# Kernel tuning notes

Measured on AMD Instinct MI355X. Metric: run time of the kernel, lower is better.

The kernel has to match this reference:

```python
import jax, jax.numpy as jnp
import numpy as np

B, S, HID = 1, 2048, 2048
H, KV, D = 16, 4, 128
N_REP = H // KV
WINDOW = 1024
THETA = 10000.0
EPS = 1e-6
SCALE = D ** -0.5


def setup_inputs() -> dict:
    key = jax.random.key(0)
    ks = jax.random.split(key, 10)
    s = 0.02
    return {
        "hidden_states": jax.random.normal(ks[0], (B, S, HID), jnp.float32),
        "Wq": jax.random.normal(ks[1], (HID, H * D), jnp.float32) * s,
        "bq": jnp.zeros((H * D,), jnp.float32),
        "Wk": jax.random.normal(ks[2], (HID, KV * D), jnp.float32) * s,
        "bk": jnp.zeros((KV * D,), jnp.float32),
        "Wv": jax.random.normal(ks[3], (HID, KV * D), jnp.float32) * s,
        "bv": jnp.zeros((KV * D,), jnp.float32),
        "Wo": jax.random.normal(ks[4], (H * D, HID), jnp.float32) * s,
        "memory_gate": jnp.zeros((1, H, 1, 1), jnp.float32),
    }


def _rope_tables(seq_len, dim, dtype):
    inv_freq = 1.0 / (THETA ** (jnp.arange(0, dim, 2, dtype=jnp.float32) / dim))
    t = jnp.arange(seq_len, dtype=jnp.float32)
    freqs = t[:, None] * inv_freq[None, :]          # [S, D/2]
    emb = jnp.concatenate([freqs, freqs], axis=-1)  # [S, D]
    return jnp.cos(emb).astype(dtype), jnp.sin(emb).astype(dtype)


def _rotate_half(x):
    x1, x2 = x[..., : x.shape[-1] // 2], x[..., x.shape[-1] // 2 :]
    return jnp.concatenate([-x2, x1], axis=-1)


def reference(hidden_states, Wq, bq, Wk, bk, Wv, bv, Wo, memory_gate):
    b, s, _ = hidden_states.shape
    q = (hidden_states @ Wq + bq).reshape(b, s, H, D).transpose(0, 2, 1, 3)   # [B,H,S,D]
    k = (hidden_states @ Wk + bk).reshape(b, s, KV, D).transpose(0, 2, 1, 3)  # [B,KV,S,D]
    v = (hidden_states @ Wv + bv).reshape(b, s, KV, D).transpose(0, 2, 1, 3)

    cos, sin = _rope_tables(s, D, q.dtype)  # [S,D]
    cos = cos[None, None]                   # [1,1,S,D]
    sin = sin[None, None]
    q_rot = q * cos + _rotate_half(q) * sin
    k_rot = k * cos + _rotate_half(k) * sin

    # GQA repeat of rotated K and raw V to H heads
    k_rep = jnp.repeat(k_rot, N_REP, axis=1)  # [B,H,S,D]
    v_rep = jnp.repeat(v, N_REP, axis=1)

    # sliding-window causal attention (seq_len > window path)
    scores = jnp.einsum("bhsd,bhtd->bhst", q_rot, k_rep) * SCALE
    row = jnp.arange(s)[:, None]
    col = jnp.arange(s)[None, :]
    mask = (col <= row) & (row - col < WINDOW)  # [S,S]
    scores = jnp.where(mask[None, None], scores, -jnp.inf)
    probs = jax.nn.softmax(scores.astype(jnp.float32), axis=-1).astype(q.dtype)
    local = jnp.einsum("bhst,bhtd->bhsd", probs, v_rep)

    # infini-memory retrieval: memory is reset before retrieve, so M=0, z=0
    sigma_q = jax.nn.elu(q) + 1.0                        # unrotated (NoPE) query
    M = jnp.zeros((b, H, D, D), q.dtype)
    z = jnp.zeros((b, H, D), q.dtype)
    num = jnp.einsum("bhsd,bhde->bhse", sigma_q, M)
    den = jnp.einsum("bhsd,bhd->bhs", sigma_q, z) + EPS
    global_out = num / den[..., None]                    # zeros, but faithful math

    gate = jax.nn.sigmoid(memory_gate)                   # [1,H,1,1]
    out = gate * global_out + (1.0 - gate) * local       # [B,H,S,D]
    out = out.transpose(0, 2, 1, 3).reshape(b, s, H * D)
    return out @ Wo
```

## Files before the change

kernel.cpp:

```cpp
#include <hip/hip_runtime.h>
#include <stdint.h>

typedef __attribute__((ext_vector_type(8))) short short8;
typedef __attribute__((ext_vector_type(4))) float f32x4;

#define S_LEN 2048
#define HID 2048
#define NH 16
#define NKV 4
#define DH 128
#define WINDOW 1024
#define SCALE 0.08838834764831845f

__device__ __forceinline__ unsigned short f2bf(float f) {
    unsigned int u = __float_as_uint(f);
    unsigned int r = (u + 0x7fffu + ((u >> 16) & 1u)) >> 16;
    return (unsigned short)r;
}

__device__ __forceinline__ void gload16(const void* g, void* l) {
    __builtin_amdgcn_global_load_lds((__attribute__((address_space(1))) void*)g,
                                     (__attribute__((address_space(3))) void*)l, 16, 0, 0);
}


__device__ __forceinline__ void tile_transpose(const float* __restrict__ src,
                                               unsigned short* __restrict__ dst,
                                               int N, int K, int rowoff, int idx, int nbx,
                                               unsigned short (*t)[33]) {
    const int nx = idx & (nbx - 1), ky = idx / nbx;
    const int n0 = nx * 32, k0 = ky * 32;
    const int c = threadIdx.x & 31, r8 = threadIdx.x >> 5;
#pragma unroll
    for (int i = 0; i < 4; i++) {
        int r = r8 + i * 8;
        t[r][c] = f2bf(src[(size_t)(k0 + r) * N + n0 + c]);
    }
    __syncthreads();
#pragma unroll
    for (int i = 0; i < 4; i++) {
        int r = r8 + i * 8;
        dst[(size_t)(rowoff + n0 + r) * K + k0 + c] = t[c][r];
    }
}

__global__ __launch_bounds__(256) void prep_kernel(
    const float* __restrict__ hs, unsigned short* __restrict__ hsb,
    const float* __restrict__ bq, const float* __restrict__ bk, const float* __restrict__ bv,
    float* __restrict__ cbias, float* __restrict__ cst, float* __restrict__ snt,
    const float* __restrict__ Wq, const float* __restrict__ Wk,
    const float* __restrict__ Wv, const float* __restrict__ Wo,
    unsigned short* __restrict__ wqkvT, unsigned short* __restrict__ woT) {
    __shared__ unsigned short t[32][33];
    const int b = blockIdx.x, tid = threadIdx.x;
    if (b < 4096) {
        int i = b * 256 + tid;
        float4 v = ((const float4*)hs)[i];
        ushort4 o;
        o.x = f2bf(v.x); o.y = f2bf(v.y); o.z = f2bf(v.z); o.w = f2bf(v.w);
        ((ushort4*)hsb)[i] = o;
    } else if (b < 4608) {
        int idx = (b - 4096) * 256 + tid;
        int s = idx >> 6, f = idx & 63;
        float inv = __expf(-(float)f * (logf(10000.f) / 64.f));
        float ang = (float)s * inv;
        float si, co;
        sincosf(ang, &si, &co);
        cst[idx] = co;
        snt[idx] = si;
    } else if (b < 4620) {
        int i = (b - 4608) * 256 + tid;
        if (i < 3072) {
            float v;
            if (i < 2048) v = bq[i];
            else if (i < 2560) v = bk[i - 2048];
            else v = bv[i - 2560];
            cbias[i] = v;
        }
    } else if (b < 8716) {
        tile_transpose(Wq, wqkvT, 2048, 2048, 0, b - 4620, 64, t);
    } else if (b < 9740) {
        tile_transpose(Wk, wqkvT, 512, 2048, 2048, b - 8716, 16, t);
    } else if (b < 10764) {
        tile_transpose(Wv, wqkvT, 512, 2048, 2560, b - 9740, 16, t);
    } else {
        tile_transpose(Wo, woT, 2048, 2048, 0, b - 10764, 64, t);
    }
}


template <int EPI>
__global__ __launch_bounds__(256) void gemm_pipe(
    const unsigned short* __restrict__ A, const unsigned short* __restrict__ Bt,
    float* __restrict__ C, const float* __restrict__ bias, int M, int N, int K,
    unsigned short* __restrict__ Qr, unsigned short* __restrict__ Kr,
    unsigned short* __restrict__ Vt,
    const float* __restrict__ cst, const float* __restrict__ snt) {
    __shared__ unsigned short Al[3][128 * 32];
    __shared__ unsigned short Bl[3][128 * 32];
    const int tid = threadIdx.x, lane = tid & 63, w = tid >> 6;
    const int lo = lane & 15, hi = lane >> 4;
    const int nbn = N >> 7;
    const int nwg8 = gridDim.x >> 3;
    const int wg = (blockIdx.x & 7) * nwg8 + (blockIdx.x >> 3);
    const int bm = wg / nbn, bn = wg % nbn;
    const int m0 = bm << 7, n0 = bn << 7;
    const size_t Kb = (size_t)K * 2;

    const char* Ab = (const char*)A + (size_t)m0 * Kb;
    const char* Bb = (const char*)Bt + (size_t)n0 * Kb;
    char* Alb = (char*)&Al[0][0];
    char* Blb = (char*)&Bl[0][0];

    const int L0 = tid * 16;
    const int L1 = 4096 + tid * 16;
    const int r0 = L0 >> 6, r1 = L1 >> 6;
    const size_t go0 = (size_t)r0 * Kb + ((((L0 >> 4) & 3) ^ (r0 & 3)) << 4);
    const size_t go1 = (size_t)r1 * Kb + ((((L1 >> 4) & 3) ^ (r1 & 3)) << 4);

    auto stage = [&](int buf, int kt) {
        const char* Ak = Ab + (size_t)kt * 64;
        const char* Bk = Bb + (size_t)kt * 64;
        char* Ad = Alb + buf * 8192;
        char* Bd = Blb + buf * 8192;
        gload16(Ak + go0, Ad + L0);
        gload16(Ak + go1, Ad + L1);
        gload16(Bk + go0, Bd + L0);
        gload16(Bk + go1, Bd + L1);
    };

    f32x4 acc[2][8] = {};
    const int NT = K >> 5;
    const int swz = (hi ^ (lo & 3)) << 4;

    stage(0, 0);
    stage(1, 1);
    int buf = 0, nstage = 2;
    for (int kt = 0; kt < NT; ++kt) {
        if (kt < NT - 1)
            asm volatile("s_waitcnt vmcnt(4)" ::: "memory");
        else
            asm volatile("s_waitcnt vmcnt(0)" ::: "memory");
        __builtin_amdgcn_s_barrier();

        const char* Ar = Alb + buf * 8192;
        const char* Br = Blb + buf * 8192;
        short8 af[2], bfr[8];
#pragma unroll
        for (int m = 0; m < 2; m++)
            af[m] = *(const short8*)(Ar + (w * 32 + m * 16 + lo) * 64 + swz);
#pragma unroll
        for (int n = 0; n < 8; n++)
            bfr[n] = *(const short8*)(Br + (n * 16 + lo) * 64 + swz);
        asm volatile("s_waitcnt lgkmcnt(0)" ::: "memory");
        __builtin_amdgcn_s_barrier();

        if (kt + 2 < NT) {
            int bst = nstage;
            bst = (bst >= 3) ? bst - 3 : bst;
            stage(bst, kt + 2);
            nstage = bst + 1;
        }
        __builtin_amdgcn_sched_barrier(0);

        __builtin_amdgcn_s_setprio(1);
#pragma unroll
        for (int m = 0; m < 2; m++)
#pragma unroll
            for (int n = 0; n < 8; n++)
                acc[m][n] = __builtin_amdgcn_mfma_f32_16x16x32_bf16(af[m], bfr[n], acc[m][n], 0, 0, 0);
        __builtin_amdgcn_s_setprio(0);

        buf = (buf == 2) ? 0 : buf + 1;
    }

    const int sbase = m0 + w * 32 + hi * 4;
    if constexpr (EPI == 0) {
#pragma unroll
        for (int m = 0; m < 2; m++) {
            const int row = sbase + m * 16;
#pragma unroll
            for (int n = 0; n < 8; n++) {
                const int col = n0 + n * 16 + lo;
                const float badd = bias ? bias[col] : 0.f;
#pragma unroll
                for (int r = 0; r < 4; r++)
                    C[(size_t)(row + r) * N + col] = acc[m][n][r] + badd;
            }
        }
    } else {
        if (bn < 20) {
            float csv[2][4][4], snv[2][4][4];
#pragma unroll
            for (int m = 0; m < 2; m++)
#pragma unroll
                for (int r = 0; r < 4; r++) {
                    const int s = sbase + m * 16 + r;
#pragma unroll
                    for (int fi = 0; fi < 4; fi++) {
                        const int f = fi * 16 + lo;
                        csv[m][r][fi] = cst[s * 64 + f];
                        snv[m][r][fi] = snt[s * 64 + f];
                    }
                }
            unsigned short* dst = (bn < 16) ? (Qr + (size_t)bn * S_LEN * 128)
                                            : (Kr + (size_t)(bn - 16) * S_LEN * 128);
#pragma unroll
            for (int m = 0; m < 2; m++) {
#pragma unroll
                for (int n = 0; n < 8; n++) {
                    const int d = n * 16 + lo;
                    const float badd = bias[n0 + d];
                    const float badd2 = bias[n0 + (d ^ 64)];
#pragma unroll
                    for (int r = 0; r < 4; r++) {
                        const float x = acc[m][n][r] + badd;
                        const float y = acc[m][n ^ 4][r] + badd2;
                        const float cs = csv[m][r][n & 3];
                        const float sn = snv[m][r][n & 3];
                        const float out = (n < 4) ? x * cs - y * sn : x * cs + y * sn;
                        const int s = sbase + m * 16 + r;
                        dst[(size_t)s * 128 + d] = f2bf(out);
                    }
                }
            }
        } else {
            const int kvh = bn - 20;
#pragma unroll
            for (int m = 0; m < 2; m++) {
                const int s0r = sbase + m * 16;
#pragma unroll
                for (int n = 0; n < 8; n++) {
                    const int d = n * 16 + lo;
                    const float badd = bias[n0 + d];
                    ushort4 pk;
                    pk.x = f2bf(acc[m][n][0] + badd);
                    pk.y = f2bf(acc[m][n][1] + badd);
                    pk.z = f2bf(acc[m][n][2] + badd);
                    pk.w = f2bf(acc[m][n][3] + badd);
                    *(ushort4*)(Vt + (size_t)(kvh * 128 + d) * S_LEN + s0r) = pk;
                }
            }
        }
    }
}


__global__ __launch_bounds__(256) void attn_kernel(const unsigned short* __restrict__ Qr,
                                                   const unsigned short* __restrict__ Kr,
                                                   const unsigned short* __restrict__ Vt,
                                                   const float* __restrict__ mg,
                                                   unsigned short* __restrict__ Ao) {
    __shared__ unsigned short Kl[2][64 * 128];
    __shared__ unsigned short Vl[2][128 * 64];
    __shared__ unsigned short Pl[4][16 * 64];
    const int tid = threadIdx.x, lane = tid & 63, w = tid >> 6;
    const int h = blockIdx.y, qt = blockIdx.x;
    const int kvh = h >> 2;
    const int q0 = qt * 64;
    const int lo = lane & 15, hi = lane >> 4;

    const unsigned short* Qb =
        Qr + ((size_t)h * S_LEN + q0 + w * 16 + lo) * 128 + hi * 8;
    short8 qf[4];
#pragma unroll
    for (int ks = 0; ks < 4; ++ks) qf[ks] = *(const short8*)(Qb + ks * 32);

    const float gate = 1.f / (1.f + __expf(-mg[h]));
    const float fac = 1.f - gate;

    const short8 ones = {16256, 16256, 16256, 16256, 16256, 16256, 16256, 16256};

    float mrow[4] = {-INFINITY, -INFINITY, -INFINITY, -INFINITY};
    f32x4 o[8] = {};
    f32x4 ol = {};

    const char* Kg = (const char*)(Kr + (size_t)kvh * S_LEN * 128);
    const char* Vg = (const char*)(Vt + (size_t)kvh * 128 * S_LEN);
    char* Klb = (char*)&Kl[0][0];
    char* Vlb = (char*)&Vl[0][0];
    const int wb = w * 1024;

    auto stage = [&](int buf, int kt) {
        const int k0 = kt * 64;
#pragma unroll
        for (int iss = 0; iss < 4; ++iss) {
            int lin = iss * 4096 + tid * 16;
            int row = lin >> 8;
            int chunk = (lin >> 4) & 15;
            gload16(Kg + (size_t)(k0 + row) * 256 + ((chunk ^ (row & 7)) << 4),
                    Klb + buf * 16384 + iss * 4096 + wb);
            int d = lin >> 7;
            int vchunk = (lin >> 4) & 7;
            gload16(Vg + (size_t)d * (S_LEN * 2) + (size_t)k0 * 2 + ((vchunk ^ (d & 7)) << 4),
                    Vlb + buf * 16384 + iss * 4096 + wb);
        }
    };

    const int qmin = q0 + w * 16;
    const int t0 = (q0 >= 1023) ? (q0 - 1023) >> 6 : 0;
    stage(0, t0);
    for (int kt = t0; kt <= qt; ++kt) {
        __syncthreads();
        if (kt < qt) stage((kt - t0 + 1) & 1, kt + 1);
        const int buf = (kt - t0) & 1;
        const int k0 = kt * 64;
        const char* Kb = Klb + buf * 16384;
        const char* Vb = Vlb + buf * 16384;

        f32x4 sc[4];
        __builtin_amdgcn_s_setprio(1);
#pragma unroll
        for (int t = 0; t < 4; t++) {
            sc[t] = (f32x4){0.f, 0.f, 0.f, 0.f};
            const int krow = t * 16 + lo;
#pragma unroll
            for (int ks = 0; ks < 4; ks++) {
                const int chunk = ks * 4 + hi;
                short8 kf = *(const short8*)(Kb + krow * 256 + ((chunk ^ (krow & 7)) << 4));
                sc[t] = __builtin_amdgcn_mfma_f32_16x16x32_bf16(qf[ks], kf, sc[t], 0, 0, 0);
            }
        }
        __builtin_amdgcn_s_setprio(0);

        const bool full = (k0 + 63 <= qmin) && (k0 >= qmin + 15 - (WINDOW - 1));
        float ps[4][4];
        float mt[4];
        if (full) {
#pragma unroll
            for (int r = 0; r < 4; r++) {
                float m0v = -INFINITY;
#pragma unroll
                for (int t = 0; t < 4; t++) {
                    float sv = sc[t][r] * SCALE;
                    ps[t][r] = sv;
                    m0v = fmaxf(m0v, sv);
                }
                mt[r] = m0v;
            }
        } else {
#pragma unroll
            for (int r = 0; r < 4; r++) {
                const int q = qmin + hi * 4 + r;
                float m0v = -INFINITY;
#pragma unroll
                for (int t = 0; t < 4; t++) {
                    const int k = k0 + t * 16 + lo;
                    const bool valid = (k <= q) && (q - k < WINDOW);
                    float sv = valid ? sc[t][r] * SCALE : -INFINITY;
                    ps[t][r] = sv;
                    m0v = fmaxf(m0v, sv);
                }
                mt[r] = m0v;
            }
        }

        float alpha[4];
        bool need = false;
#pragma unroll
        for (int r = 0; r < 4; r++) {
#pragma unroll
            for (int off = 1; off < 16; off <<= 1) mt[r] = fmaxf(mt[r], __shfl_xor(mt[r], off, 64));
            const float mo = mrow[r];
            const float mn = (mt[r] > mo + 8.f) ? mt[r] : mo;
            const bool resc = (mn != mo);
            alpha[r] = resc ? __expf(mo - mn) : 1.f;
            need = need || resc;
            mrow[r] = mn;
            const float mn_e = (mn == -INFINITY) ? 0.f : mn;
#pragma unroll
            for (int t = 0; t < 4; t++) ps[t][r] = __expf(ps[t][r] - mn_e);
        }

        char* Pw = (char*)&Pl[w][0];
#pragma unroll
        for (int r = 0; r < 4; r++) {
            const int prow = hi * 4 + r;
#pragma unroll
            for (int t = 0; t < 4; t++) {
                const int col = t * 16 + lo;
                const int chunk = col >> 3;
                *(unsigned short*)(Pw + prow * 128 + ((chunk ^ (prow & 7)) << 4) + (col & 7) * 2) =
                    f2bf(ps[t][r]);
            }
        }
        asm volatile("s_waitcnt lgkmcnt(0)" ::: "memory");
        __builtin_amdgcn_sched_barrier(0);

        if (__any(need)) {
#pragma unroll
            for (int n = 0; n < 8; n++)
#pragma unroll
                for (int r = 0; r < 4; r++) o[n][r] *= alpha[r];
#pragma unroll
            for (int r = 0; r < 4; r++) ol[r] *= alpha[r];
        }

        short8 pa[2];
#pragma unroll
        for (int ks = 0; ks < 2; ++ks) {
            const int chunk = ks * 4 + hi;
            pa[ks] = *(const short8*)(Pw + lo * 128 + ((chunk ^ (lo & 7)) << 4));
        }

        __builtin_amdgcn_s_setprio(1);
        ol = __builtin_amdgcn_mfma_f32_16x16x32_bf16(pa[0], ones, ol, 0, 0, 0);
        ol = __builtin_amdgcn_mfma_f32_16x16x32_bf16(pa[1], ones, ol, 0, 0, 0);
#pragma unroll
        for (int n = 0; n < 8; n++) {
            const int d = n * 16 + lo;
#pragma unroll
            for (int ks = 0; ks < 2; ++ks) {
                const int chunk = ks * 4 + hi;
                short8 vbf = *(const short8*)(Vb + d * 128 + ((chunk ^ (d & 7)) << 4));
                o[n] = __builtin_amdgcn_mfma_f32_16x16x32_bf16(pa[ks], vbf, o[n], 0, 0, 0);
            }
        }
        __builtin_amdgcn_s_setprio(0);
        __syncthreads();
    }

#pragma unroll
    for (int r = 0; r < 4; r++) {
        const int s = q0 + w * 16 + hi * 4 + r;
        const float inv = fac / ol[r];
#pragma unroll
        for (int n = 0; n < 8; n++) {
            const int d = n * 16 + lo;
            Ao[(size_t)s * 2048 + h * 128 + d] = f2bf(o[n][r] * inv);
        }
    }
}


extern "C" void kernel_launch(void* const* d_in, const int* in_sizes, int n_in,
                              void* d_out, int out_size, void* d_ws, size_t ws_size,
                              hipStream_t stream) {
    const float* hs = (const float*)d_in[0];
    const float* Wq = (const float*)d_in[1];
    const float* bq = (const float*)d_in[2];
    const float* Wk = (const float*)d_in[3];
    const float* bk = (const float*)d_in[4];
    const float* Wv = (const float*)d_in[5];
    const float* bv = (const float*)d_in[6];
    const float* Wo = (const float*)d_in[7];
    const float* mg = (const float*)d_in[8];

    char* ws = (char*)d_ws;
    unsigned short* hsb   = (unsigned short*)(ws + 0);
    unsigned short* attnb = (unsigned short*)(ws + 0);
    unsigned short* wqkvT = (unsigned short*)(ws + 8388608);
    unsigned short* woT   = (unsigned short*)(ws + 20971520);
    unsigned short* Qrb   = (unsigned short*)(ws + 29360128);
    unsigned short* Krb   = (unsigned short*)(ws + 37748736);
    unsigned short* Vtb   = (unsigned short*)(ws + 39845888);
    float*          cbias = (float*)(ws + 41943040);
    float*          cst   = (float*)(ws + 41959424);
    float*          snt   = (float*)(ws + 42483712);

    prep_kernel<<<14860, 256, 0, stream>>>(hs, hsb, bq, bk, bv, cbias, cst, snt,
                                           Wq, Wk, Wv, Wo, wqkvT, woT);

    gemm_pipe<1><<<16 * 24, 256, 0, stream>>>(hsb, wqkvT, nullptr, cbias, 2048, 3072, 2048,
                                              Qrb, Krb, Vtb, cst, snt);

    attn_kernel<<<dim3(32, 16), 256, 0, stream>>>(Qrb, Krb, Vtb, mg, attnb);

    gemm_pipe<0><<<16 * 16, 256, 0, stream>>>(attnb, woT, (float*)d_out, nullptr, 2048, 2048, 2048,
                                              nullptr, nullptr, nullptr, nullptr, nullptr);
}
```

Measured before the change: 235.1 us.

## Split attention KV range across two blocks with merge kernel; widen weight transposes

Result: slower. 248.4 us (+5.6%).

```diff
diff --git a/kernel.cpp b/kernel.cpp
--- a/kernel.cpp
+++ b/kernel.cpp
@@ -10,7 +10,7 @@
 #define NKV 4
 #define DH 128
 #define WINDOW 1024
-#define SCALE 0.08838834764831845f
+#define SCALE2 0.12751744f
 
 __device__ __forceinline__ unsigned short f2bf(float f) {
     unsigned int u = __float_as_uint(f);
@@ -24,23 +24,32 @@
 }
 
 
-__device__ __forceinline__ void tile_transpose(const float* __restrict__ src,
-                                               unsigned short* __restrict__ dst,
-                                               int N, int K, int rowoff, int idx, int nbx,
-                                               unsigned short (*t)[33]) {
-    const int nx = idx & (nbx - 1), ky = idx / nbx;
-    const int n0 = nx * 32, k0 = ky * 32;
-    const int c = threadIdx.x & 31, r8 = threadIdx.x >> 5;
-#pragma unroll
-    for (int i = 0; i < 4; i++) {
-        int r = r8 + i * 8;
-        t[r][c] = f2bf(src[(size_t)(k0 + r) * N + n0 + c]);
+__device__ __forceinline__ void tile_t64(const float* __restrict__ src,
+                                         unsigned short* __restrict__ dst,
+                                         int N, int K, int rowoff, int idx, int nbx,
+                                         unsigned short* t ) {
+    const int nx = idx % nbx, ky = idx / nbx;
+    const int n0 = nx * 64, k0 = ky * 64;
+    const int tid = threadIdx.x;
+#pragma unroll
+    for (int it = 0; it < 4; it++) {
+        const int id = it * 256 + tid;
+        const int k = id >> 4, nc = (id & 15) * 4;
+        float4 v = *(const float4*)(src + (size_t)(k0 + k) * N + n0 + nc);
+        ushort4 o;
+        o.x = f2bf(v.x); o.y = f2bf(v.y); o.z = f2bf(v.z); o.w = f2bf(v.w);
+        *(ushort4*)&t[k * 72 + (nc ^ ((k >> 3) << 3))] = o;
     }
     __syncthreads();
 #pragma unroll
-    for (int i = 0; i < 4; i++) {
-        int r = r8 + i * 8;
-        dst[(size_t)(rowoff + n0 + r) * K + k0 + c] = t[c][r];
+    for (int it = 0; it < 2; it++) {
+        const int id = it * 256 + tid;
+        const int n = id >> 3, kc = (id & 7) * 8;
+        const int cswz = n ^ ((id & 7) << 3);
+        short8 v;
+#pragma unroll
+        for (int j = 0; j < 8; j++) v[j] = (short)t[(kc + j) * 72 + cswz];
+        *(short8*)(dst + (size_t)(rowoff + n0 + n) * K + k0 + kc) = v;
     }
 }
 
@@ -51,25 +60,27 @@
     const float* __restrict__ Wq, const float* __restrict__ Wk,
     const float* __restrict__ Wv, const float* __restrict__ Wo,
     unsigned short* __restrict__ wqkvT, unsigned short* __restrict__ woT) {
-    __shared__ unsigned short t[32][33];
+    __shared__ unsigned short t[64 * 72];
     const int b = blockIdx.x, tid = threadIdx.x;
-    if (b < 4096) {
-        int i = b * 256 + tid;
-        float4 v = ((const float4*)hs)[i];
-        ushort4 o;
-        o.x = f2bf(v.x); o.y = f2bf(v.y); o.z = f2bf(v.z); o.w = f2bf(v.w);
-        ((ushort4*)hsb)[i] = o;
-    } else if (b < 4608) {
-        int idx = (b - 4096) * 256 + tid;
-        int s = idx >> 6, f = idx & 63;
+    if (b < 2048) {
+        const int i = b * 256 + tid;
+        float4 v0 = ((const float4*)hs)[i * 2];
+        float4 v1 = ((const float4*)hs)[i * 2 + 1];
+        short8 o;
+        o[0] = f2bf(v0.x); o[1] = f2bf(v0.y); o[2] = f2bf(v0.z); o[3] = f2bf(v0.w);
+        o[4] = f2bf(v1.x); o[5] = f2bf(v1.y); o[6] = f2bf(v1.z); o[7] = f2bf(v1.w);
+        ((short8*)hsb)[i] = o;
+    } else if (b < 2560) {
+        const int idx = (b - 2048) * 256 + tid;
+        const int s = idx >> 6, f = idx & 63;
         float inv = __expf(-(float)f * (logf(10000.f) / 64.f));
         float ang = (float)s * inv;
         float si, co;
         sincosf(ang, &si, &co);
         cst[idx] = co;
         snt[idx] = si;
-    } else if (b < 4620) {
-        int i = (b - 4608) * 256 + tid;
+    } else if (b < 2572) {
+        const int i = (b - 2560) * 256 + tid;
         if (i < 3072) {
             float v;
             if (i < 2048) v = bq[i];
@@ -77,14 +88,14 @@
             else v = bv[i - 2560];
             cbias[i] = v;
         }
-    } else if (b < 8716) {
-        tile_transpose(Wq, wqkvT, 2048, 2048, 0, b - 4620, 64, t);
-    } else if (b < 9740) {
-        tile_transpose(Wk, wqkvT, 512, 2048, 2048, b - 8716, 16, t);
-    } else if (b < 10764) {
-        tile_transpose(Wv, wqkvT, 512, 2048, 2560, b - 9740, 16, t);
+    } else if (b < 3596) {
+        tile_t64(Wq, wqkvT, 2048, 2048, 0, b - 2572, 32, t);
+    } else if (b < 3852) {
+        tile_t64(Wk, wqkvT, 512, 2048, 2048, b - 3596, 8, t);
+    } else if (b < 4108) {
+        tile_t64(Wv, wqkvT, 512, 2048, 2560, b - 3852, 8, t);
     } else {
-        tile_transpose(Wo, woT, 2048, 2048, 0, b - 10764, 64, t);
+        tile_t64(Wo, woT, 2048, 2048, 0, b - 4108, 32, t);
     }
 }
 
@@ -249,25 +260,40 @@
 __global__ __launch_bounds__(256) void attn_kernel(const unsigned short* __restrict__ Qr,
                                                    const unsigned short* __restrict__ Kr,
                                                    const unsigned short* __restrict__ Vt,
-                                                   const float* __restrict__ mg,
-                                                   unsigned short* __restrict__ Ao) {
+                                                   float* __restrict__ Op,
+                                                   float2* __restrict__ mlb) {
     __shared__ unsigned short Kl[2][64 * 128];
     __shared__ unsigned short Vl[2][128 * 64];
     __shared__ unsigned short Pl[4][16 * 64];
     const int tid = threadIdx.x, lane = tid & 63, w = tid >> 6;
-    const int h = blockIdx.y, qt = blockIdx.x;
+    const int h = blockIdx.y, qt = blockIdx.x, z = blockIdx.z;
     const int kvh = h >> 2;
     const int q0 = qt * 64;
     const int lo = lane & 15, hi = lane >> 4;
 
+    const int t0f = (q0 >= 1023) ? (q0 - 1023) >> 6 : 0;
+    const int T = qt - t0f + 1;
+    const int half = T >> 1;
+    const int tb = z ? t0f + half : t0f;
+    const int te = z ? qt : t0f + half - 1;
+    const int zh = z * 16 + h;
+
+    if (te < tb) {
+        if (lo == 0) {
+#pragma unroll
+            for (int r = 0; r < 4; r++) {
+                const int s = q0 + w * 16 + hi * 4 + r;
+                mlb[(size_t)zh * S_LEN + s] = make_float2(-INFINITY, 0.f);
+            }
+        }
+        return;
+    }
+
     const unsigned short* Qb =
         Qr + ((size_t)h * S_LEN + q0 + w * 16 + lo) * 128 + hi * 8;
     short8 qf[4];
 #pragma unroll
     for (int ks = 0; ks < 4; ++ks) qf[ks] = *(const short8*)(Qb + ks * 32);
-
-    const float gate = 1.f / (1.f + __expf(-mg[h]));
-    const float fac = 1.f - gate;
 
     const short8 ones = {16256, 16256, 16256, 16256, 16256, 16256, 16256, 16256};
 
@@ -298,12 +324,11 @@
     };
 
     const int qmin = q0 + w * 16;
-    const int t0 = (q0 >= 1023) ? (q0 - 1023) >> 6 : 0;
-    stage(0, t0);
-    for (int kt = t0; kt <= qt; ++kt) {
+    stage(0, tb);
+    for (int kt = tb; kt <= te; ++kt) {
         __syncthreads();
-        if (kt < qt) stage((kt - t0 + 1) & 1, kt + 1);
-        const int buf = (kt - t0) & 1;
+        if (kt < te) stage((kt - tb + 1) & 1, kt + 1);
+        const int buf = (kt - tb) & 1;
         const int k0 = kt * 64;
         const char* Kb = Klb + buf * 16384;
         const char* Vb = Vlb + buf * 16384;
@@ -332,7 +357,7 @@
                 float m0v = -INFINITY;
 #pragma unroll
                 for (int t = 0; t < 4; t++) {
-                    float sv = sc[t][r] * SCALE;
+                    float sv = sc[t][r] * SCALE2;
                     ps[t][r] = sv;
                     m0v = fmaxf(m0v, sv);
                 }
@@ -347,7 +372,7 @@
                 for (int t = 0; t < 4; t++) {
                     const int k = k0 + t * 16 + lo;
                     const bool valid = (k <= q) && (q - k < WINDOW);
-                    float sv = valid ? sc[t][r] * SCALE : -INFINITY;
+                    float sv = valid ? sc[t][r] * SCALE2 : -INFINITY;
                     ps[t][r] = sv;
                     m0v = fmaxf(m0v, sv);
                 }
@@ -364,12 +389,12 @@
             const float mo = mrow[r];
             const float mn = (mt[r] > mo + 8.f) ? mt[r] : mo;
             const bool resc = (mn != mo);
-            alpha[r] = resc ? __expf(mo - mn) : 1.f;
+            alpha[r] = resc ? exp2f(mo - mn) : 1.f;
             need = need || resc;
             mrow[r] = mn;
             const float mn_e = (mn == -INFINITY) ? 0.f : mn;
 #pragma unroll
-            for (int t = 0; t < 4; t++) ps[t][r] = __expf(ps[t][r] - mn_e);
+            for (int t = 0; t < 4; t++) ps[t][r] = exp2f(ps[t][r] - mn_e);
         }
 
         char* Pw = (char*)&Pl[w][0];
@@ -420,16 +445,56 @@
         __syncthreads();
     }
 
+    float* Ob = Op + ((size_t)zh * S_LEN + q0 + w * 16) * 128;
 #pragma unroll
     for (int r = 0; r < 4; r++) {
-        const int s = q0 + w * 16 + hi * 4 + r;
-        const float inv = fac / ol[r];
+        const int sq = hi * 4 + r;
 #pragma unroll
         for (int n = 0; n < 8; n++) {
             const int d = n * 16 + lo;
-            Ao[(size_t)s * 2048 + h * 128 + d] = f2bf(o[n][r] * inv);
-        }
-    }
+            Ob[(size_t)sq * 128 + d] = o[n][r];
+        }
+    }
+    if (lo == 0) {
+#pragma unroll
+        for (int r = 0; r < 4; r++) {
+            const int s = q0 + w * 16 + hi * 4 + r;
+            mlb[(size_t)zh * S_LEN + s] = make_float2(mrow[r], ol[r]);
+        }
+    }
+}
+
+
+__global__ __launch_bounds__(256) void merge_kernel(const float* __restrict__ Op,
+                                                    const float2* __restrict__ mlb,
+                                                    const float* __restrict__ mg,
+                                                    unsigned short* __restrict__ attnb) {
+    const int s = blockIdx.x;
+    const int h = threadIdx.x >> 4;
+    const int d0 = (threadIdx.x & 15) * 8;
+    const float fac = 1.f - 1.f / (1.f + __expf(-mg[h]));
+    const float2 a = mlb[(size_t)h * S_LEN + s];
+    const float2 b = mlb[(size_t)(16 + h) * S_LEN + s];
+    const float m0 = (a.y > 0.f) ? a.x : -INFINITY;
+    const float m1 = (b.y > 0.f) ? b.x : -INFINITY;
+    const float ms = fmaxf(m0, m1);
+    const float c0 = (a.y > 0.f) ? exp2f(a.x - ms) : 0.f;
+    const float c1 = (b.y > 0.f) ? exp2f(b.x - ms) : 0.f;
+    const float inv = fac / (c0 * a.y + c1 * b.y);
+    const float* O0 = Op + ((size_t)h * S_LEN + s) * 128 + d0;
+    const float* O1 = Op + ((size_t)(16 + h) * S_LEN + s) * 128 + d0;
+    float4 x0 = *(const float4*)O0, x1 = *(const float4*)(O0 + 4);
+    float4 y0 = *(const float4*)O1, y1 = *(const float4*)(O1 + 4);
+    short8 out;
+    out[0] = f2bf((c0 * x0.x + c1 * y0.x) * inv);
+    out[1] = f2bf((c0 * x0.y + c1 * y0.y) * inv);
+    out[2] = f2bf((c0 * x0.z + c1 * y0.z) * inv);
+    out[3] = f2bf((c0 * x0.w + c1 * y0.w) * inv);
+    out[4] = f2bf((c0 * x1.x + c1 * y1.x) * inv);
+    out[5] = f2bf((c0 * x1.y + c1 * y1.y) * inv);
+    out[6] = f2bf((c0 * x1.z + c1 * y1.z) * inv);
+    out[7] = f2bf((c0 * x1.w + c1 * y1.w) * inv);
+    *(short8*)(attnb + (size_t)s * 2048 + h * 128 + d0) = out;
 }
 
 
@@ -447,24 +512,28 @@
     const float* mg = (const float*)d_in[8];
 
     char* ws = (char*)d_ws;
+    float*          Op    = (float*)(ws + 0);
     unsigned short* hsb   = (unsigned short*)(ws + 0);
-    unsigned short* attnb = (unsigned short*)(ws + 0);
     unsigned short* wqkvT = (unsigned short*)(ws + 8388608);
-    unsigned short* woT   = (unsigned short*)(ws + 20971520);
-    unsigned short* Qrb   = (unsigned short*)(ws + 29360128);
-    unsigned short* Krb   = (unsigned short*)(ws + 37748736);
-    unsigned short* Vtb   = (unsigned short*)(ws + 39845888);
-    float*          cbias = (float*)(ws + 41943040);
-    float*          cst   = (float*)(ws + 41959424);
-    float*          snt   = (float*)(ws + 42483712);
-
-    prep_kernel<<<14860, 256, 0, stream>>>(hs, hsb, bq, bk, bv, cbias, cst, snt,
-                                           Wq, Wk, Wv, Wo, wqkvT, woT);
+    unsigned short* Qrb   = (unsigned short*)(ws + 33554432);
+    unsigned short* Krb   = (unsigned short*)(ws + 41943040);
+    unsigned short* Vtb   = (unsigned short*)(ws + 44040192);
+    unsigned short* woT   = (unsigned short*)(ws + 46137344);
+    float*          cbias = (float*)(ws + 54525952);
+    float*          cst   = (float*)(ws + 54542336);
+    float*          snt   = (float*)(ws + 55066624);
+    float2*         mlb   = (float2*)(ws + 55590912);
+    unsigned short* attnb = (unsigned short*)(ws + 56623104);
+
+    prep_kernel<<<5132, 256, 0, stream>>>(hs, hsb, bq, bk, bv, cbias, cst, snt,
+                                          Wq, Wk, Wv, Wo, wqkvT, woT);
 
     gemm_pipe<1><<<16 * 24, 256, 0, stream>>>(hsb, wqkvT, nullptr, cbias, 2048, 3072, 2048,
                                               Qrb, Krb, Vtb, cst, snt);
 
-    attn_kernel<<<dim3(32, 16), 256, 0, stream>>>(Qrb, Krb, Vtb, mg, attnb);
+    attn_kernel<<<dim3(32, 16, 2), 256, 0, stream>>>(Qrb, Krb, Vtb, Op, mlb);
+
+    merge_kernel<<<2048, 256, 0, stream>>>(Op, mlb, mg, attnb);
 
     gemm_pipe<0><<<16 * 16, 256, 0, stream>>>(attnb, woT, (float*)d_out, nullptr, 2048, 2048, 2048,
                                               nullptr, nullptr, nullptr, nullptr, nullptr);
```
